# Kernel tuning notes

Hardware: AMD Instinct MI355X
Metric: run time of the kernel (lower is better)

Reference implementation:

```python
import jax, jax.numpy as jnp
import numpy as np

N_NODES = 20000
N_EDGES = 640000


def graph_conv(x, src, dst, W, b, n_nodes):
    """DGL GraphConv with norm='both': D_in^{-1/2} A D_out^{-1/2} X W + b."""
    ones = jnp.ones(src.shape[0], dtype=x.dtype)
    deg_out = jnp.maximum(jax.ops.segment_sum(ones, src, num_segments=n_nodes), 1.0)
    deg_in = jnp.maximum(jax.ops.segment_sum(ones, dst, num_segments=n_nodes), 1.0)
    xs = x * (deg_out ** -0.5)[:, None]          # scale src features
    agg = jax.ops.segment_sum(xs[src], dst, num_segments=n_nodes)  # [N, d]
    agg = agg * (deg_in ** -0.5)[:, None]
    return agg @ W + b


def setup_inputs() -> dict:
    key = jax.random.key(0)
    ks = jax.random.split(key, 10)
    d = 256
    scale = 1.0 / np.sqrt(d)
    return {
        "x": jax.random.normal(ks[0], (N_NODES, d), dtype=jnp.float32),
        "side_src": jax.random.randint(ks[1], (N_EDGES,), 0, N_NODES),
        "side_dst": jax.random.randint(ks[2], (N_EDGES,), 0, N_NODES),
        "upd_src": jax.random.randint(ks[3], (N_EDGES,), 0, N_NODES),
        "upd_dst": jax.random.randint(ks[4], (N_EDGES,), 0, N_NODES),
        "W1_side": jax.random.normal(ks[5], (d, d), dtype=jnp.float32) * scale,
        "b1_side": jnp.zeros((d,), dtype=jnp.float32),
        "W1_upd": jax.random.normal(ks[6], (d, d), dtype=jnp.float32) * scale,
        "b1_upd": jnp.zeros((d,), dtype=jnp.float32),
        "W2_side": jax.random.normal(ks[7], (d, d), dtype=jnp.float32) * scale,
        "b2_side": jnp.zeros((d,), dtype=jnp.float32),
        "W2_upd": jax.random.normal(ks[8], (d, d), dtype=jnp.float32) * scale,
        "b2_upd": jnp.zeros((d,), dtype=jnp.float32),
    }


def reference(x, side_src, side_dst, upd_src, upd_dst,
              W1_side, b1_side, W1_upd, b1_upd,
              W2_side, b2_side, W2_upd, b2_upd):
    n = x.shape[0]
    # layer 1: HeteroGraphConv with aggregate='sum' over relations, then relu
    h = (graph_conv(x, side_src, side_dst, W1_side, b1_side, n)
         + graph_conv(x, upd_src, upd_dst, W1_upd, b1_upd, n))
    h = jax.nn.relu(h)
    # layer 2
    out = (graph_conv(h, side_src, side_dst, W2_side, b2_side, n)
           + graph_conv(h, upd_src, upd_dst, W2_upd, b2_upd, n))
    return out
```

## Files before the change

### kernel.cpp

```cpp
#include <hip/hip_runtime.h>

typedef __attribute__((ext_vector_type(8))) short short8;
typedef __attribute__((ext_vector_type(4))) float f32x4;

#define SCHUNK 2048
#define MAXN   20480
#define NSLICE 8
#define NPB    40

__device__ inline unsigned short f2bf(float v) {
    unsigned u = __float_as_uint(v);
    u += 0x7FFFu + ((u >> 16) & 1u);
    return (unsigned short)(u >> 16);
}
__device__ inline float bf2f(unsigned short h) {
    return __uint_as_float((unsigned)h << 16);
}

__global__ void bias_sum_kernel(const float* __restrict__ b1s, const float* __restrict__ b1u,
                                const float* __restrict__ b2s, const float* __restrict__ b2u,
                                float* __restrict__ bsum1, float* __restrict__ bsum2) {
    int i = threadIdx.x;
    bsum1[i] = b1s[i] + b1u[i];
    bsum2[i] = b2s[i] + b2u[i];
}

__global__ void wprep_kernel(const float* __restrict__ W1s, const float* __restrict__ W1u,
                             const float* __restrict__ W2s, const float* __restrict__ W2u,
                             unsigned short* __restrict__ Bpk1, unsigned short* __restrict__ Bpk2) {
    int k = blockIdx.x;
    int nn = threadIdx.x;
    int layer = blockIdx.y;
    const float* Ws = layer ? W2s : W1s;
    const float* Wu = layer ? W2u : W1u;
    float w = (k < 256) ? Ws[k * 256 + nn] : Wu[(k - 256) * 256 + nn];
    unsigned short hi = f2bf(w);
    unsigned short lo = f2bf(w - bf2f(hi));
    unsigned short* B = layer ? Bpk2 : Bpk1;
    size_t frag = ((size_t)(nn >> 4) * 16 + (k >> 5)) * 2;
    size_t addr = frag * 512 + ((nn & 15) + ((k >> 3) & 3) * 16) * 8 + (k & 7);
    B[addr] = hi;
    B[addr + 512] = lo;
}

__global__ __launch_bounds__(256) void hist_kernel(
    const int* __restrict__ sS, const int* __restrict__ dS,
    const int* __restrict__ sU, const int* __restrict__ dU,
    int Es, int Eu, int n, int nblk, unsigned int* __restrict__ histG) {
    __shared__ unsigned int h[MAXN];
    const int rel = blockIdx.y;
    const int* src = rel ? sU : sS;
    const int* dst = rel ? dU : dS;
    int E = rel ? Eu : Es;
    int b = blockIdx.x;
    int chunk = (E + nblk - 1) / nblk;
    int beg = b * chunk;
    int end = min(E, beg + chunk);
    for (int i = threadIdx.x; i < n; i += 256) h[i] = 0u;
    __syncthreads();
    for (int i = beg + threadIdx.x; i < end; i += 256) {
        atomicAdd(&h[src[i]], 1u);
        atomicAdd(&h[dst[i]], 0x10000u);
    }
    __syncthreads();
    unsigned int* out = histG + ((size_t)rel * nblk + b) * n;
    for (int i = threadIdx.x; i < n; i += 256) out[i] = h[i];
}

__global__ void totals_kernel(const unsigned int* __restrict__ histG, int n, int nblk,
                              float* __restrict__ sOutS, float* __restrict__ sInS,
                              float* __restrict__ sOutU, float* __restrict__ sInU,
                              int* __restrict__ degInS, int* __restrict__ degInU) {
    const int rel = blockIdx.y;
    int i = blockIdx.x * 256 + threadIdx.x;
    if (i >= n) return;
    const unsigned int* hg = histG + (size_t)rel * nblk * n + i;
    unsigned int lo = 0, hi = 0;
    int b = 0;
    for (; b + 8 <= nblk; b += 8) {
        unsigned v0 = hg[(size_t)(b + 0) * n];
        unsigned v1 = hg[(size_t)(b + 1) * n];
        unsigned v2 = hg[(size_t)(b + 2) * n];
        unsigned v3 = hg[(size_t)(b + 3) * n];
        unsigned v4 = hg[(size_t)(b + 4) * n];
        unsigned v5 = hg[(size_t)(b + 5) * n];
        unsigned v6 = hg[(size_t)(b + 6) * n];
        unsigned v7 = hg[(size_t)(b + 7) * n];
        lo += (v0 & 0xFFFFu) + (v1 & 0xFFFFu) + (v2 & 0xFFFFu) + (v3 & 0xFFFFu)
            + (v4 & 0xFFFFu) + (v5 & 0xFFFFu) + (v6 & 0xFFFFu) + (v7 & 0xFFFFu);
        hi += (v0 >> 16) + (v1 >> 16) + (v2 >> 16) + (v3 >> 16)
            + (v4 >> 16) + (v5 >> 16) + (v6 >> 16) + (v7 >> 16);
    }
    for (; b < nblk; ++b) {
        unsigned v = hg[(size_t)b * n];
        lo += v & 0xFFFFu;
        hi += v >> 16;
    }
    float so = rsqrtf((float)(lo > 1u ? lo : 1u));
    float si = rsqrtf((float)(hi > 1u ? hi : 1u));
    if (rel) { sOutU[i] = so; sInU[i] = si; degInU[i] = (int)hi; }
    else     { sOutS[i] = so; sInS[i] = si; degInS[i] = (int)hi; }
}

__global__ __launch_bounds__(256) void scan_part_kernel(const int* __restrict__ degA,
                                                        const int* __restrict__ degB,
                                                        int n, int NB, int* __restrict__ bsum) {
    const int rel = blockIdx.y;
    const int* deg = rel ? degB : degA;
    int t = threadIdx.x;
    int base = blockIdx.x * SCHUNK + t * 8;
    int s = 0;
    if (base + 8 <= n) {
        int4 a = *(const int4*)(deg + base);
        int4 b = *(const int4*)(deg + base + 4);
        s = a.x + a.y + a.z + a.w + b.x + b.y + b.z + b.w;
    } else {
        for (int i = 0; i < 8; ++i)
            if (base + i < n) s += deg[base + i];
    }
    __shared__ int sm[256];
    sm[t] = s;
    __syncthreads();
    for (int off = 128; off > 0; off >>= 1) {
        if (t < off) sm[t] += sm[t + off];
        __syncthreads();
    }
    if (t == 0) bsum[rel * NB + blockIdx.x] = sm[0];
}

__global__ void scan_mid_kernel(int* __restrict__ bsum, int NB,
                                int* __restrict__ rpA, int* __restrict__ rpB, int n) {
    int t = threadIdx.x;
    if (t >= 2) return;
    int* bs = bsum + t * NB;
    int run = 0;
    for (int i = 0; i < NB; ++i) {
        int v = bs[i];
        bs[i] = run;
        run += v;
    }
    int* rp = t ? rpB : rpA;
    rp[n] = run;
}

__global__ __launch_bounds__(256) void scan_final_kernel(const int* __restrict__ degA,
                                                         const int* __restrict__ degB,
                                                         const int* __restrict__ bsum,
                                                         int n, int NB,
                                                         int* __restrict__ rpA,
                                                         int* __restrict__ rpB) {
    const int rel = blockIdx.y;
    const int* deg = rel ? degB : degA;
    int* rp = rel ? rpB : rpA;
    int t = threadIdx.x;
    int base = blockIdx.x * SCHUNK + t * 8;
    int v[8];
    if (base + 8 <= n) {
        int4 a = *(const int4*)(deg + base);
        int4 b = *(const int4*)(deg + base + 4);
        v[0] = a.x; v[1] = a.y; v[2] = a.z; v[3] = a.w;
        v[4] = b.x; v[5] = b.y; v[6] = b.z; v[7] = b.w;
    } else {
        for (int i = 0; i < 8; ++i) v[i] = (base + i < n) ? deg[base + i] : 0;
    }
    int s = 0;
    #pragma unroll
    for (int i = 0; i < 8; ++i) s += v[i];
    __shared__ int sm[256];
    sm[t] = s;
    __syncthreads();
    #pragma unroll
    for (int off = 1; off < 256; off <<= 1) {
        int y = (t >= off) ? sm[t - off] : 0;
        __syncthreads();
        sm[t] += y;
        __syncthreads();
    }
    int run = bsum[rel * NB + blockIdx.x] + sm[t] - s;
    #pragma unroll
    for (int i = 0; i < 8; ++i) {
        if (base + i < n) rp[base + i] = run;
        run += v[i];
    }
}

__global__ void offsets_kernel(const unsigned int* __restrict__ histG,
                               const int* __restrict__ rpS, const int* __restrict__ rpU,
                               int n, int nblk, int* __restrict__ offsG) {
    const int rel = blockIdx.y;
    int i = blockIdx.x * 256 + threadIdx.x;
    if (i >= n) return;
    const unsigned int* hg = histG + (size_t)rel * nblk * n + i;
    int* og = offsG + (size_t)rel * nblk * n + i;
    int run = (rel ? rpU : rpS)[i];
    int b = 0;
    for (; b + 8 <= nblk; b += 8) {
        unsigned v0 = hg[(size_t)(b + 0) * n];
        unsigned v1 = hg[(size_t)(b + 1) * n];
        unsigned v2 = hg[(size_t)(b + 2) * n];
        unsigned v3 = hg[(size_t)(b + 3) * n];
        unsigned v4 = hg[(size_t)(b + 4) * n];
        unsigned v5 = hg[(size_t)(b + 5) * n];
        unsigned v6 = hg[(size_t)(b + 6) * n];
        unsigned v7 = hg[(size_t)(b + 7) * n];
        og[(size_t)(b + 0) * n] = run; run += (int)(v0 >> 16);
        og[(size_t)(b + 1) * n] = run; run += (int)(v1 >> 16);
        og[(size_t)(b + 2) * n] = run; run += (int)(v2 >> 16);
        og[(size_t)(b + 3) * n] = run; run += (int)(v3 >> 16);
        og[(size_t)(b + 4) * n] = run; run += (int)(v4 >> 16);
        og[(size_t)(b + 5) * n] = run; run += (int)(v5 >> 16);
        og[(size_t)(b + 6) * n] = run; run += (int)(v6 >> 16);
        og[(size_t)(b + 7) * n] = run; run += (int)(v7 >> 16);
    }
    for (; b < nblk; ++b) {
        unsigned v = hg[(size_t)b * n];
        og[(size_t)b * n] = run;
        run += (int)(v >> 16);
    }
}

__global__ __launch_bounds__(256) void csr_scatter_kernel(
    const int* __restrict__ sS, const int* __restrict__ dS,
    const int* __restrict__ sU, const int* __restrict__ dU,
    int Es, int Eu, int n, int nblk, const int* __restrict__ offsG,
    const float* __restrict__ sOutS, const float* __restrict__ sOutU,
    int2* __restrict__ csrPS, int2* __restrict__ csrPU) {
    __shared__ int off[MAXN];
    const int rel = blockIdx.y;
    const int* src = rel ? sU : sS;
    const int* dst = rel ? dU : dS;
    const float* so = rel ? sOutU : sOutS;
    int2* csrP = rel ? csrPU : csrPS;
    int E = rel ? Eu : Es;
    int b = blockIdx.x;
    int chunk = (E + nblk - 1) / nblk;
    int beg = b * chunk;
    int end = min(E, beg + chunk);
    const int* og = offsG + ((size_t)rel * nblk + b) * n;
    for (int i = threadIdx.x; i < n; i += 256) off[i] = og[i];
    __syncthreads();
    for (int i = beg + threadIdx.x; i < end; i += 256) {
        int s = src[i];
        int pos = atomicAdd(&off[dst[i]], 1);
        csrP[pos] = make_int2(s, __float_as_int(so[s]));
    }
}

__global__ __launch_bounds__(256) void pull_slice_kernel(
    const float4* __restrict__ xin,
    const int2* __restrict__ csrPS, const int2* __restrict__ csrPU,
    const int* __restrict__ rpS, const int* __restrict__ rpU,
    const float* __restrict__ sinS, const float* __restrict__ sinU,
    unsigned short* __restrict__ aggPk, int n) {
    __shared__ int2 elds[4][64];
    int bid = blockIdx.x;
    int slice = bid & (NSLICE - 1);
    int rest = bid >> 3;
    int rel = rest & 1;
    int chunk = rest >> 1;
    const int2* csrP = rel ? csrPU : csrPS;
    const int* rp = rel ? rpU : rpS;
    const float* sinv = rel ? sinU : sinS;

    int wave = threadIdx.x >> 6;
    int lane = threadIdx.x & 63;
    int sub = lane >> 3;
    int sl = lane & 7;
    int fbase = slice * 8 + sl;
    int kstepg = rel * 8 + slice;

    int start = chunk * NPB;
    int lim = min(n, start + NPB);
    int node = start + wave;
    if (node >= lim) return;

    int beg = rp[node], end = rp[node + 1];
    {
        int cnt = min(end - beg, 64);
        int2 p = make_int2(0, 0);
        if (lane < cnt) p = csrP[beg + lane];
        elds[wave][lane] = p;
    }
    const int2* ebase = &elds[wave][sub];

    while (node < lim) {
        int next = node + 4;
        int nbeg = 0, nend = 0;
        int2 np = make_int2(0, 0);
        if (next < lim) {
            nbeg = rp[next];
            nend = rp[next + 1];
            int ncnt = min(nend - nbeg, 64);
            if (lane < ncnt) np = csrP[nbeg + lane];
        }
        float ax = 0.f, ay = 0.f, az = 0.f, aw = 0.f;
        int cnt = min(end - beg, 64);
        int jmax = (cnt + 7) >> 3;
        int j = 0;
        for (; j + 4 <= jmax; j += 4) {
            int2 e0 = ebase[(j + 0) * 8];
            int2 e1 = ebase[(j + 1) * 8];
            int2 e2 = ebase[(j + 2) * 8];
            int2 e3 = ebase[(j + 3) * 8];
            float4 a0 = xin[(size_t)e0.x * 64 + fbase];
            float4 a1 = xin[(size_t)e1.x * 64 + fbase];
            float4 a2 = xin[(size_t)e2.x * 64 + fbase];
            float4 a3 = xin[(size_t)e3.x * 64 + fbase];
            float w0 = __int_as_float(e0.y), w1 = __int_as_float(e1.y);
            float w2 = __int_as_float(e2.y), w3 = __int_as_float(e3.y);
            ax += w0 * a0.x + w1 * a1.x + w2 * a2.x + w3 * a3.x;
            ay += w0 * a0.y + w1 * a1.y + w2 * a2.y + w3 * a3.y;
            az += w0 * a0.z + w1 * a1.z + w2 * a2.z + w3 * a3.z;
            aw += w0 * a0.w + w1 * a1.w + w2 * a2.w + w3 * a3.w;
        }
        for (; j < jmax; ++j) {
            int2 e = ebase[j * 8];
            float4 a = xin[(size_t)e.x * 64 + fbase];
            float w = __int_as_float(e.y);
            ax += w * a.x; ay += w * a.y; az += w * a.z; aw += w * a.w;
        }
        for (int eb = beg + 64; eb < end; eb += 64) {
            int scnt = end - eb;
            if (scnt > 64) scnt = 64;
            int myu = 0;
            float myw = 0.f;
            if (lane < scnt) {
                int2 p = csrP[eb + lane];
                myu = p.x;
                myw = __int_as_float(p.y);
            }
            int sjmax = (scnt + 7) >> 3;
            for (int sj = 0; sj < sjmax; ++sj) {
                int idx = sj * 8 + sub;
                int u = __shfl(myu, idx);
                float w = __shfl(myw, idx);
                float4 a = xin[(size_t)u * 64 + fbase];
                ax += w * a.x; ay += w * a.y; az += w * a.z; aw += w * a.w;
            }
        }
        ax += __shfl_xor(ax, 8);  ax += __shfl_xor(ax, 16); ax += __shfl_xor(ax, 32);
        ay += __shfl_xor(ay, 8);  ay += __shfl_xor(ay, 16); ay += __shfl_xor(ay, 32);
        az += __shfl_xor(az, 8);  az += __shfl_xor(az, 16); az += __shfl_xor(az, 32);
        aw += __shfl_xor(aw, 8);  aw += __shfl_xor(aw, 16); aw += __shfl_xor(aw, 32);
        if (sub == 0) {
            float si = sinv[node];
            float vx = si * ax, vy = si * ay, vz = si * az, vw = si * aw;
            ushort4 hi4 = make_ushort4(f2bf(vx), f2bf(vy), f2bf(vz), f2bf(vw));
            ushort4 lo4 = make_ushort4(f2bf(vx - bf2f(hi4.x)), f2bf(vy - bf2f(hi4.y)),
                                       f2bf(vz - bf2f(hi4.z)), f2bf(vw - bf2f(hi4.w)));
            size_t frag = ((size_t)(node >> 4) * 16 + kstepg) * 2;
            size_t addr = frag * 512 + ((node & 15) + (sl >> 1) * 16) * 8 + (sl & 1) * 4;
            *(ushort4*)&aggPk[addr] = hi4;
            *(ushort4*)&aggPk[addr + 512] = lo4;
        }
        if (next < lim) elds[wave][lane] = np;
        beg = nbeg;
        end = nend;
        node = next;
    }
}

template <int RELU>
__global__ __launch_bounds__(512) void gemm_mfma_kernel(
    const short8* __restrict__ Apk, const short8* __restrict__ Bpk,
    const float* __restrict__ bias, float* __restrict__ C, int M) {
    __shared__ short8 lds[2][42][64];
    int tid = threadIdx.x;
    int lane = tid & 63;
    int wv = tid >> 6;
    int mt0 = blockIdx.x * 5;
    int m0 = blockIdx.x * 80;
    if (m0 >= M) return;
    int nt0 = wv * 2;
    int col0 = wv * 32;
    int frow = lane & 15;

    int sf[6], sln[6];
    bool sv[6];
    #pragma unroll
    for (int r = 0; r < 6; ++r) {
        int s = r * 512 + tid;
        sv[r] = s < 2688;
        sf[r] = s >> 6;
        sln[r] = s & 63;
    }
    auto gaddr = [&](int f, int l, int ks) -> size_t {
        if (f < 10) {
            return ((size_t)(mt0 + (f >> 1)) * 16 + ks) * 128 + (f & 1) * 64 + l;
        } else {
            int q = f - 10;
            return ((size_t)(q >> 1) * 16 + ks) * 128 + (q & 1) * 64 + l;
        }
    };

    f32x4 acc[5][2];
    #pragma unroll
    for (int fr = 0; fr < 5; ++fr)
        #pragma unroll
        for (int fc = 0; fc < 2; ++fc)
            acc[fr][fc] = (f32x4){0.f, 0.f, 0.f, 0.f};

    short8 stg[6];
    #pragma unroll
    for (int r = 0; r < 6; ++r)
        if (sv[r]) stg[r] = (sf[r] < 10 ? Apk : Bpk)[gaddr(sf[r], sln[r], 0)];
    #pragma unroll
    for (int r = 0; r < 6; ++r)
        if (sv[r]) lds[0][sf[r]][sln[r]] = stg[r];
    __syncthreads();

    int cur = 0;
    for (int ks = 0; ks < 16; ++ks) {
        if (ks + 1 < 16) {
            #pragma unroll
            for (int r = 0; r < 6; ++r)
                if (sv[r]) stg[r] = (sf[r] < 10 ? Apk : Bpk)[gaddr(sf[r], sln[r], ks + 1)];
        }
        short8 bh[2], bl[2];
        #pragma unroll
        for (int fc = 0; fc < 2; ++fc) {
            bh[fc] = lds[cur][10 + (nt0 + fc) * 2 + 0][lane];
            bl[fc] = lds[cur][10 + (nt0 + fc) * 2 + 1][lane];
        }
        #pragma unroll
        for (int fr = 0; fr < 5; ++fr) {
            short8 ah = lds[cur][fr * 2 + 0][lane];
            short8 al = lds[cur][fr * 2 + 1][lane];
            #pragma unroll
            for (int fc = 0; fc < 2; ++fc) {
                acc[fr][fc] = __builtin_amdgcn_mfma_f32_16x16x32_bf16(ah, bh[fc], acc[fr][fc], 0, 0, 0);
                acc[fr][fc] = __builtin_amdgcn_mfma_f32_16x16x32_bf16(al, bh[fc], acc[fr][fc], 0, 0, 0);
                acc[fr][fc] = __builtin_amdgcn_mfma_f32_16x16x32_bf16(ah, bl[fc], acc[fr][fc], 0, 0, 0);
            }
        }
        if (ks + 1 < 16) {
            #pragma unroll
            for (int r = 0; r < 6; ++r)
                if (sv[r]) lds[cur ^ 1][sf[r]][sln[r]] = stg[r];
            __syncthreads();
            cur ^= 1;
        }
    }

    #pragma unroll
    for (int fr = 0; fr < 5; ++fr)
        #pragma unroll
        for (int fc = 0; fc < 2; ++fc) {
            int c = col0 + fc * 16 + frow;
            float bc = bias[c];
            int rb = m0 + fr * 16 + (lane >> 4) * 4;
            #pragma unroll
            for (int j = 0; j < 4; ++j) {
                int r = rb + j;
                if (r < M) {
                    float v = acc[fr][fc][j] + bc;
                    if (RELU) v = fmaxf(v, 0.f);
                    C[(size_t)r * 256 + c] = v;
                }
            }
        }
}

extern "C" void kernel_launch(void* const* d_in, const int* in_sizes, int n_in,
                              void* d_out, int out_size, void* d_ws, size_t ws_size,
                              hipStream_t stream) {
    const float* x   = (const float*)d_in[0];
    const int* sS    = (const int*)d_in[1];
    const int* dS    = (const int*)d_in[2];
    const int* sU    = (const int*)d_in[3];
    const int* dU    = (const int*)d_in[4];
    const float* W1s = (const float*)d_in[5];
    const float* b1s = (const float*)d_in[6];
    const float* W1u = (const float*)d_in[7];
    const float* b1u = (const float*)d_in[8];
    const float* W2s = (const float*)d_in[9];
    const float* b2s = (const float*)d_in[10];
    const float* W2u = (const float*)d_in[11];
    const float* b2u = (const float*)d_in[12];
    float* out = (float*)d_out;

    const int n  = in_sizes[0] / 256;
    const int Es = in_sizes[1];
    const int Eu = in_sizes[3];
    const int NB = (n + SCHUNK - 1) / SCHUNK;
    const int gemmGrid = (n + 79) / 80;
    const size_t AGG_BYTES = (size_t)((n + 15) / 16 + 16) * 16 * 2 * 512 * 2;
    const size_t BPK_BYTES = (size_t)16 * 16 * 2 * 512 * 2;

    auto plan = [&](int nb) -> size_t {
        size_t t = 0;
        auto add = [&](size_t b) { t = (t + 255) & ~(size_t)255; t += b; };
        add((size_t)2 * nb * n * 4);
        add((size_t)2 * nb * n * 4);
        add((size_t)(n + 1) * 4); add((size_t)(n + 1) * 4);
        add((size_t)n * 4); add((size_t)n * 4); add((size_t)n * 4); add((size_t)n * 4);
        add((size_t)n * 4); add((size_t)n * 4);
        add(256 * 4); add(256 * 4);
        add((size_t)2 * NB * 4);
        add((size_t)Es * 8); add((size_t)Eu * 8);
        add(2 * BPK_BYTES);
        add(AGG_BYTES);
        add((size_t)n * 256 * 4);
        return t;
    };
    const int nblk = (plan(128) <= ws_size) ? 128 : 32;

    char* ws = (char*)d_ws;
    size_t off = 0;
    auto alloc = [&](size_t bytes) -> void* {
        off = (off + 255) & ~(size_t)255;
        void* p = ws + off;
        off += bytes;
        return p;
    };

    unsigned int* histG = (unsigned int*)alloc((size_t)2 * nblk * n * 4);
    int* offsG   = (int*)alloc((size_t)2 * nblk * n * 4);
    int* rpS     = (int*)alloc((size_t)(n + 1) * 4);
    int* rpU     = (int*)alloc((size_t)(n + 1) * 4);
    float* sOutS = (float*)alloc((size_t)n * 4);
    float* sInS  = (float*)alloc((size_t)n * 4);
    float* sOutU = (float*)alloc((size_t)n * 4);
    float* sInU  = (float*)alloc((size_t)n * 4);
    int* degInS  = (int*)alloc((size_t)n * 4);
    int* degInU  = (int*)alloc((size_t)n * 4);
    float* bsum1 = (float*)alloc(256 * 4);
    float* bsum2 = (float*)alloc(256 * 4);
    int* bsumBlk = (int*)alloc((size_t)2 * NB * 4);
    int2* csrPS  = (int2*)alloc((size_t)Es * 8);
    int2* csrPU  = (int2*)alloc((size_t)Eu * 8);
    unsigned short* Bpk1 = (unsigned short*)alloc(2 * BPK_BYTES);
    unsigned short* Bpk2 = Bpk1 + BPK_BYTES / 2;
    unsigned short* aggPk = (unsigned short*)alloc(AGG_BYTES);
    float* h     = (float*)alloc((size_t)n * 256 * 4);

    bias_sum_kernel<<<1, 256, 0, stream>>>(b1s, b1u, b2s, b2u, bsum1, bsum2);
    wprep_kernel<<<dim3(512, 2), 256, 0, stream>>>(W1s, W1u, W2s, W2u, Bpk1, Bpk2);
    dim3 hg(nblk, 2);
    hist_kernel<<<hg, 256, 0, stream>>>(sS, dS, sU, dU, Es, Eu, n, nblk, histG);
    dim3 tg((n + 255) / 256, 2);
    totals_kernel<<<tg, 256, 0, stream>>>(histG, n, nblk, sOutS, sInS, sOutU, sInU,
                                          degInS, degInU);
    dim3 sg(NB, 2);
    scan_part_kernel<<<sg, 256, 0, stream>>>(degInS, degInU, n, NB, bsumBlk);
    scan_mid_kernel<<<1, 64, 0, stream>>>(bsumBlk, NB, rpS, rpU, n);
    scan_final_kernel<<<sg, 256, 0, stream>>>(degInS, degInU, bsumBlk, n, NB, rpS, rpU);
    offsets_kernel<<<tg, 256, 0, stream>>>(histG, rpS, rpU, n, nblk, offsG);
    csr_scatter_kernel<<<hg, 256, 0, stream>>>(sS, dS, sU, dU, Es, Eu, n, nblk, offsG,
                                               sOutS, sOutU, csrPS, csrPU);

    int chunks = (n + NPB - 1) / NPB;
    int pullGrid = NSLICE * 2 * chunks;
    const float4* x4 = (const float4*)x;
    const float4* h4 = (const float4*)h;
    const short8* A8 = (const short8*)aggPk;
    const short8* B81 = (const short8*)Bpk1;
    const short8* B82 = (const short8*)Bpk2;

    pull_slice_kernel<<<pullGrid, 256, 0, stream>>>(x4, csrPS, csrPU, rpS, rpU,
                                                    sInS, sInU, aggPk, n);
    gemm_mfma_kernel<1><<<gemmGrid, 512, 0, stream>>>(A8, B81, bsum1, h, n);
    pull_slice_kernel<<<pullGrid, 256, 0, stream>>>(h4, csrPS, csrPU, rpS, rpU,
                                                    sInS, sInU, aggPk, n);
    gemm_mfma_kernel<0><<<gemmGrid, 512, 0, stream>>>(A8, B82, bsum2, out, n);
}
```

Baseline: 457.2 us.

## Fuse preprocessing kernels, simplify scan, and read edges directly in pull kernel

Folds the bias-sum into the weight-prep kernel and the scan partial sums into the totals kernel, which removes two launches. The scan now uses 256-node chunks instead of 2048. The pull kernel drops the LDS edge staging and prefetch of the next node's edges and reads CSR pairs straight from global memory, using padded edge arrays to allow a masked tail load. The histogram block count is halved, trading fewer partial histograms for more atomic contention per block.

```diff
diff --git a/kernel.cpp b/kernel.cpp
--- a/kernel.cpp
+++ b/kernel.cpp
@@ -3,7 +3,6 @@
 typedef __attribute__((ext_vector_type(8))) short short8;
 typedef __attribute__((ext_vector_type(4))) float f32x4;
 
-#define SCHUNK 2048
 #define MAXN   20480
 #define NSLICE 8
 #define NPB    40
@@ -17,20 +16,19 @@
     return __uint_as_float((unsigned)h << 16);
 }
 
-__global__ void bias_sum_kernel(const float* __restrict__ b1s, const float* __restrict__ b1u,
-                                const float* __restrict__ b2s, const float* __restrict__ b2u,
-                                float* __restrict__ bsum1, float* __restrict__ bsum2) {
-    int i = threadIdx.x;
-    bsum1[i] = b1s[i] + b1u[i];
-    bsum2[i] = b2s[i] + b2u[i];
-}
-
 __global__ void wprep_kernel(const float* __restrict__ W1s, const float* __restrict__ W1u,
                              const float* __restrict__ W2s, const float* __restrict__ W2u,
-                             unsigned short* __restrict__ Bpk1, unsigned short* __restrict__ Bpk2) {
+                             const float* __restrict__ b1s, const float* __restrict__ b1u,
+                             const float* __restrict__ b2s, const float* __restrict__ b2u,
+                             unsigned short* __restrict__ Bpk1, unsigned short* __restrict__ Bpk2,
+                             float* __restrict__ bsum1, float* __restrict__ bsum2) {
     int k = blockIdx.x;
     int nn = threadIdx.x;
     int layer = blockIdx.y;
+    if (k == 0) {
+        if (layer) bsum2[nn] = b2s[nn] + b2u[nn];
+        else       bsum1[nn] = b1s[nn] + b1u[nn];
+    }
     const float* Ws = layer ? W2s : W1s;
     const float* Wu = layer ? W2u : W1u;
     float w = (k < 256) ? Ws[k * 256 + nn] : Wu[(k - 256) * 256 + nn];
@@ -67,107 +65,80 @@
     for (int i = threadIdx.x; i < n; i += 256) out[i] = h[i];
 }
 
-__global__ void totals_kernel(const unsigned int* __restrict__ histG, int n, int nblk,
-                              float* __restrict__ sOutS, float* __restrict__ sInS,
-                              float* __restrict__ sOutU, float* __restrict__ sInU,
-                              int* __restrict__ degInS, int* __restrict__ degInU) {
+__global__ __launch_bounds__(256) void totals_kernel(
+    const unsigned int* __restrict__ histG, int n, int nblk,
+    float* __restrict__ sOutS, float* __restrict__ sInS,
+    float* __restrict__ sOutU, float* __restrict__ sInU,
+    int* __restrict__ degInS, int* __restrict__ degInU,
+    int* __restrict__ chunkSum ) {
     const int rel = blockIdx.y;
     int i = blockIdx.x * 256 + threadIdx.x;
-    if (i >= n) return;
-    const unsigned int* hg = histG + (size_t)rel * nblk * n + i;
     unsigned int lo = 0, hi = 0;
-    int b = 0;
-    for (; b + 8 <= nblk; b += 8) {
-        unsigned v0 = hg[(size_t)(b + 0) * n];
-        unsigned v1 = hg[(size_t)(b + 1) * n];
-        unsigned v2 = hg[(size_t)(b + 2) * n];
-        unsigned v3 = hg[(size_t)(b + 3) * n];
-        unsigned v4 = hg[(size_t)(b + 4) * n];
-        unsigned v5 = hg[(size_t)(b + 5) * n];
-        unsigned v6 = hg[(size_t)(b + 6) * n];
-        unsigned v7 = hg[(size_t)(b + 7) * n];
-        lo += (v0 & 0xFFFFu) + (v1 & 0xFFFFu) + (v2 & 0xFFFFu) + (v3 & 0xFFFFu)
-            + (v4 & 0xFFFFu) + (v5 & 0xFFFFu) + (v6 & 0xFFFFu) + (v7 & 0xFFFFu);
-        hi += (v0 >> 16) + (v1 >> 16) + (v2 >> 16) + (v3 >> 16)
-            + (v4 >> 16) + (v5 >> 16) + (v6 >> 16) + (v7 >> 16);
-    }
-    for (; b < nblk; ++b) {
-        unsigned v = hg[(size_t)b * n];
-        lo += v & 0xFFFFu;
-        hi += v >> 16;
-    }
-    float so = rsqrtf((float)(lo > 1u ? lo : 1u));
-    float si = rsqrtf((float)(hi > 1u ? hi : 1u));
-    if (rel) { sOutU[i] = so; sInU[i] = si; degInU[i] = (int)hi; }
-    else     { sOutS[i] = so; sInS[i] = si; degInS[i] = (int)hi; }
-}
-
-__global__ __launch_bounds__(256) void scan_part_kernel(const int* __restrict__ degA,
-                                                        const int* __restrict__ degB,
-                                                        int n, int NB, int* __restrict__ bsum) {
-    const int rel = blockIdx.y;
-    const int* deg = rel ? degB : degA;
+    if (i < n) {
+        const unsigned int* hg = histG + (size_t)rel * nblk * n + i;
+        int b = 0;
+        for (; b + 8 <= nblk; b += 8) {
+            unsigned v0 = hg[(size_t)(b + 0) * n];
+            unsigned v1 = hg[(size_t)(b + 1) * n];
+            unsigned v2 = hg[(size_t)(b + 2) * n];
+            unsigned v3 = hg[(size_t)(b + 3) * n];
+            unsigned v4 = hg[(size_t)(b + 4) * n];
+            unsigned v5 = hg[(size_t)(b + 5) * n];
+            unsigned v6 = hg[(size_t)(b + 6) * n];
+            unsigned v7 = hg[(size_t)(b + 7) * n];
+            lo += (v0 & 0xFFFFu) + (v1 & 0xFFFFu) + (v2 & 0xFFFFu) + (v3 & 0xFFFFu)
+                + (v4 & 0xFFFFu) + (v5 & 0xFFFFu) + (v6 & 0xFFFFu) + (v7 & 0xFFFFu);
+            hi += (v0 >> 16) + (v1 >> 16) + (v2 >> 16) + (v3 >> 16)
+                + (v4 >> 16) + (v5 >> 16) + (v6 >> 16) + (v7 >> 16);
+        }
+        for (; b < nblk; ++b) {
+            unsigned v = hg[(size_t)b * n];
+            lo += v & 0xFFFFu;
+            hi += v >> 16;
+        }
+        float so = rsqrtf((float)(lo > 1u ? lo : 1u));
+        float si = rsqrtf((float)(hi > 1u ? hi : 1u));
+        if (rel) { sOutU[i] = so; sInU[i] = si; degInU[i] = (int)hi; }
+        else     { sOutS[i] = so; sInS[i] = si; degInS[i] = (int)hi; }
+    }
+    __shared__ int sm[256];
     int t = threadIdx.x;
-    int base = blockIdx.x * SCHUNK + t * 8;
-    int s = 0;
-    if (base + 8 <= n) {
-        int4 a = *(const int4*)(deg + base);
-        int4 b = *(const int4*)(deg + base + 4);
-        s = a.x + a.y + a.z + a.w + b.x + b.y + b.z + b.w;
-    } else {
-        for (int i = 0; i < 8; ++i)
-            if (base + i < n) s += deg[base + i];
-    }
-    __shared__ int sm[256];
-    sm[t] = s;
+    sm[t] = (i < n) ? (int)hi : 0;
     __syncthreads();
     for (int off = 128; off > 0; off >>= 1) {
         if (t < off) sm[t] += sm[t + off];
         __syncthreads();
     }
-    if (t == 0) bsum[rel * NB + blockIdx.x] = sm[0];
-}
-
-__global__ void scan_mid_kernel(int* __restrict__ bsum, int NB,
-                                int* __restrict__ rpA, int* __restrict__ rpB, int n) {
+    if (t == 0) chunkSum[rel * gridDim.x + blockIdx.x] = sm[0];
+}
+
+__global__ void scan_mid_kernel(int* __restrict__ chunkSum, int NCH,
+                                int* __restrict__ rpS, int* __restrict__ rpU, int n) {
     int t = threadIdx.x;
     if (t >= 2) return;
-    int* bs = bsum + t * NB;
+    int* cs = chunkSum + t * NCH;
     int run = 0;
-    for (int i = 0; i < NB; ++i) {
-        int v = bs[i];
-        bs[i] = run;
+    for (int i = 0; i < NCH; ++i) {
+        int v = cs[i];
+        cs[i] = run;
         run += v;
     }
-    int* rp = t ? rpB : rpA;
+    int* rp = t ? rpU : rpS;
     rp[n] = run;
 }
 
-__global__ __launch_bounds__(256) void scan_final_kernel(const int* __restrict__ degA,
-                                                         const int* __restrict__ degB,
-                                                         const int* __restrict__ bsum,
-                                                         int n, int NB,
-                                                         int* __restrict__ rpA,
-                                                         int* __restrict__ rpB) {
+__global__ __launch_bounds__(256) void scan_final_kernel(
+    const int* __restrict__ degInS, const int* __restrict__ degInU,
+    const int* __restrict__ chunkPfx, int n,
+    int* __restrict__ rpS, int* __restrict__ rpU) {
     const int rel = blockIdx.y;
-    const int* deg = rel ? degB : degA;
-    int* rp = rel ? rpB : rpA;
+    const int* deg = rel ? degInU : degInS;
+    int* rp = rel ? rpU : rpS;
     int t = threadIdx.x;
-    int base = blockIdx.x * SCHUNK + t * 8;
-    int v[8];
-    if (base + 8 <= n) {
-        int4 a = *(const int4*)(deg + base);
-        int4 b = *(const int4*)(deg + base + 4);
-        v[0] = a.x; v[1] = a.y; v[2] = a.z; v[3] = a.w;
-        v[4] = b.x; v[5] = b.y; v[6] = b.z; v[7] = b.w;
-    } else {
-        for (int i = 0; i < 8; ++i) v[i] = (base + i < n) ? deg[base + i] : 0;
-    }
-    int s = 0;
-    #pragma unroll
-    for (int i = 0; i < 8; ++i) s += v[i];
+    int i = blockIdx.x * 256 + t;
+    int v = (i < n) ? deg[i] : 0;
     __shared__ int sm[256];
-    sm[t] = s;
+    sm[t] = v;
     __syncthreads();
     #pragma unroll
     for (int off = 1; off < 256; off <<= 1) {
@@ -176,12 +147,7 @@
         sm[t] += y;
         __syncthreads();
     }
-    int run = bsum[rel * NB + blockIdx.x] + sm[t] - s;
-    #pragma unroll
-    for (int i = 0; i < 8; ++i) {
-        if (base + i < n) rp[base + i] = run;
-        run += v[i];
-    }
+    if (i < n) rp[i] = chunkPfx[rel * gridDim.x + blockIdx.x] + sm[t] - v;
 }
 
 __global__ void offsets_kernel(const unsigned int* __restrict__ histG,
@@ -233,6 +199,7 @@
     int2* csrP = rel ? csrPU : csrPS;
     int E = rel ? Eu : Es;
     int b = blockIdx.x;
+    if (b == 0 && threadIdx.x < 64) csrP[E + threadIdx.x] = make_int2(0, 0);
     int chunk = (E + nblk - 1) / nblk;
     int beg = b * chunk;
     int end = min(E, beg + chunk);
@@ -252,7 +219,6 @@
     const int* __restrict__ rpS, const int* __restrict__ rpU,
     const float* __restrict__ sinS, const float* __restrict__ sinU,
     unsigned short* __restrict__ aggPk, int n) {
-    __shared__ int2 elds[4][64];
     int bid = blockIdx.x;
     int slice = bid & (NSLICE - 1);
     int rest = bid >> 3;
@@ -271,37 +237,18 @@
 
     int start = chunk * NPB;
     int lim = min(n, start + NPB);
-    int node = start + wave;
-    if (node >= lim) return;
-
-    int beg = rp[node], end = rp[node + 1];
-    {
-        int cnt = min(end - beg, 64);
-        int2 p = make_int2(0, 0);
-        if (lane < cnt) p = csrP[beg + lane];
-        elds[wave][lane] = p;
-    }
-    const int2* ebase = &elds[wave][sub];
-
-    while (node < lim) {
-        int next = node + 4;
-        int nbeg = 0, nend = 0;
-        int2 np = make_int2(0, 0);
-        if (next < lim) {
-            nbeg = rp[next];
-            nend = rp[next + 1];
-            int ncnt = min(nend - nbeg, 64);
-            if (lane < ncnt) np = csrP[nbeg + lane];
-        }
+    for (int node = start + wave; node < lim; node += 4) {
+        int beg = rp[node], end = rp[node + 1];
+        int deg = end - beg;
         float ax = 0.f, ay = 0.f, az = 0.f, aw = 0.f;
-        int cnt = min(end - beg, 64);
-        int jmax = (cnt + 7) >> 3;
+        const int2* ep = csrP + beg + sub;
+        int jfull = deg >> 3;
         int j = 0;
-        for (; j + 4 <= jmax; j += 4) {
-            int2 e0 = ebase[(j + 0) * 8];
-            int2 e1 = ebase[(j + 1) * 8];
-            int2 e2 = ebase[(j + 2) * 8];
-            int2 e3 = ebase[(j + 3) * 8];
+        for (; j + 4 <= jfull; j += 4) {
+            int2 e0 = ep[(j + 0) * 8];
+            int2 e1 = ep[(j + 1) * 8];
+            int2 e2 = ep[(j + 2) * 8];
+            int2 e3 = ep[(j + 3) * 8];
             float4 a0 = xin[(size_t)e0.x * 64 + fbase];
             float4 a1 = xin[(size_t)e1.x * 64 + fbase];
             float4 a2 = xin[(size_t)e2.x * 64 + fbase];
@@ -313,30 +260,18 @@
             az += w0 * a0.z + w1 * a1.z + w2 * a2.z + w3 * a3.z;
             aw += w0 * a0.w + w1 * a1.w + w2 * a2.w + w3 * a3.w;
         }
-        for (; j < jmax; ++j) {
-            int2 e = ebase[j * 8];
+        for (; j < jfull; ++j) {
+            int2 e = ep[j * 8];
             float4 a = xin[(size_t)e.x * 64 + fbase];
             float w = __int_as_float(e.y);
             ax += w * a.x; ay += w * a.y; az += w * a.z; aw += w * a.w;
         }
-        for (int eb = beg + 64; eb < end; eb += 64) {
-            int scnt = end - eb;
-            if (scnt > 64) scnt = 64;
-            int myu = 0;
-            float myw = 0.f;
-            if (lane < scnt) {
-                int2 p = csrP[eb + lane];
-                myu = p.x;
-                myw = __int_as_float(p.y);
-            }
-            int sjmax = (scnt + 7) >> 3;
-            for (int sj = 0; sj < sjmax; ++sj) {
-                int idx = sj * 8 + sub;
-                int u = __shfl(myu, idx);
-                float w = __shfl(myw, idx);
-                float4 a = xin[(size_t)u * 64 + fbase];
-                ax += w * a.x; ay += w * a.y; az += w * a.z; aw += w * a.w;
-            }
+        if (deg & 7) {
+            int idx = jfull * 8 + sub;
+            int2 e = ep[jfull * 8];
+            float w = (idx < deg) ? __int_as_float(e.y) : 0.f;
+            float4 a = xin[(size_t)e.x * 64 + fbase];
+            ax += w * a.x; ay += w * a.y; az += w * a.z; aw += w * a.w;
         }
         ax += __shfl_xor(ax, 8);  ax += __shfl_xor(ax, 16); ax += __shfl_xor(ax, 32);
         ay += __shfl_xor(ay, 8);  ay += __shfl_xor(ay, 16); ay += __shfl_xor(ay, 32);
@@ -353,10 +288,6 @@
             *(ushort4*)&aggPk[addr] = hi4;
             *(ushort4*)&aggPk[addr + 512] = lo4;
         }
-        if (next < lim) elds[wave][lane] = np;
-        beg = nbeg;
-        end = nend;
-        node = next;
     }
 }
 
@@ -482,7 +413,7 @@
     const int n  = in_sizes[0] / 256;
     const int Es = in_sizes[1];
     const int Eu = in_sizes[3];
-    const int NB = (n + SCHUNK - 1) / SCHUNK;
+    const int NCH = (n + 255) / 256;
     const int gemmGrid = (n + 79) / 80;
     const size_t AGG_BYTES = (size_t)((n + 15) / 16 + 16) * 16 * 2 * 512 * 2;
     const size_t BPK_BYTES = (size_t)16 * 16 * 2 * 512 * 2;
@@ -496,14 +427,14 @@
         add((size_t)n * 4); add((size_t)n * 4); add((size_t)n * 4); add((size_t)n * 4);
         add((size_t)n * 4); add((size_t)n * 4);
         add(256 * 4); add(256 * 4);
-        add((size_t)2 * NB * 4);
-        add((size_t)Es * 8); add((size_t)Eu * 8);
+        add((size_t)2 * NCH * 4);
+        add((size_t)(Es + 64) * 8); add((size_t)(Eu + 64) * 8);
         add(2 * BPK_BYTES);
         add(AGG_BYTES);
         add((size_t)n * 256 * 4);
         return t;
     };
-    const int nblk = (plan(128) <= ws_size) ? 128 : 32;
+    const int nblk = (plan(64) <= ws_size) ? 64 : 32;
 
     char* ws = (char*)d_ws;
     size_t off = 0;
@@ -526,25 +457,24 @@
     int* degInU  = (int*)alloc((size_t)n * 4);
     float* bsum1 = (float*)alloc(256 * 4);
     float* bsum2 = (float*)alloc(256 * 4);
-    int* bsumBlk = (int*)alloc((size_t)2 * NB * 4);
-    int2* csrPS  = (int2*)alloc((size_t)Es * 8);
-    int2* csrPU  = (int2*)alloc((size_t)Eu * 8);
+    int* chunkSum = (int*)alloc((size_t)2 * NCH * 4);
+    int2* csrPS  = (int2*)alloc((size_t)(Es + 64) * 8);
+    int2* csrPU  = (int2*)alloc((size_t)(Eu + 64) * 8);
     unsigned short* Bpk1 = (unsigned short*)alloc(2 * BPK_BYTES);
     unsigned short* Bpk2 = Bpk1 + BPK_BYTES / 2;
     unsigned short* aggPk = (unsigned short*)alloc(AGG_BYTES);
     float* h     = (float*)alloc((size_t)n * 256 * 4);
 
-    bias_sum_kernel<<<1, 256, 0, stream>>>(b1s, b1u, b2s, b2u, bsum1, bsum2);
-    wprep_kernel<<<dim3(512, 2), 256, 0, stream>>>(W1s, W1u, W2s, W2u, Bpk1, Bpk2);
+    wprep_kernel<<<dim3(512, 2), 256, 0, stream>>>(W1s, W1u, W2s, W2u,
+                                                   b1s, b1u, b2s, b2u,
+                                                   Bpk1, Bpk2, bsum1, bsum2);
     dim3 hg(nblk, 2);
     hist_kernel<<<hg, 256, 0, stream>>>(sS, dS, sU, dU, Es, Eu, n, nblk, histG);
-    dim3 tg((n + 255) / 256, 2);
+    dim3 tg(NCH, 2);
     totals_kernel<<<tg, 256, 0, stream>>>(histG, n, nblk, sOutS, sInS, sOutU, sInU,
-                                          degInS, degInU);
-    dim3 sg(NB, 2);
-    scan_part_kernel<<<sg, 256, 0, stream>>>(degInS, degInU, n, NB, bsumBlk);
-    scan_mid_kernel<<<1, 64, 0, stream>>>(bsumBlk, NB, rpS, rpU, n);
-    scan_final_kernel<<<sg, 256, 0, stream>>>(degInS, degInU, bsumBlk, n, NB, rpS, rpU);
+                                          degInS, degInU, chunkSum);
+    scan_mid_kernel<<<1, 64, 0, stream>>>(chunkSum, NCH, rpS, rpU, n);
+    scan_final_kernel<<<tg, 256, 0, stream>>>(degInS, degInU, chunkSum, n, rpS, rpU);
     offsets_kernel<<<tg, 256, 0, stream>>>(histG, rpS, rpU, n, nblk, offsG);
     csr_scatter_kernel<<<hg, 256, 0, stream>>>(sS, dS, sU, dU, Es, Eu, n, nblk, offsG,
                                                sOutS, sOutU, csrPS, csrPU);
```

Result: slower. 502.5 us (+9.9%).
